# Performance work log

Hardware: AMD Instinct MI355X
Metric: run time of the kernel (lower is better)

The kernel has to match this reference:

```python
import jax, jax.numpy as jnp
import numpy as np

B, C_IN, C_OUT, H, W = 16, 128, 256, 80, 80
K, STRIDE, PAD = 3, 2, 1
KK = K * K
HO = (H + 2 * PAD - K) // STRIDE + 1
WO = (W + 2 * PAD - K) // STRIDE + 1


def setup_inputs() -> dict:
    key = jax.random.key(0)
    ks = jax.random.split(key, 3)
    x = jax.random.normal(ks[0], (B, C_IN, H, W), jnp.float32)
    offset_w = jax.random.normal(ks[1], (2 * KK, C_IN), jnp.float32) * 0.01
    offset_b = jnp.zeros((2 * KK,), jnp.float32)
    deform_w = jax.random.normal(ks[2], (C_OUT, C_IN, K, K), jnp.float32) * (1.0 / np.sqrt(C_IN * KK))
    deform_b = jnp.zeros((C_OUT,), jnp.float32)
    bn_gamma = jnp.ones((C_OUT,), jnp.float32)
    bn_beta = jnp.zeros((C_OUT,), jnp.float32)
    return dict(x=x, offset_w=offset_w, offset_b=offset_b, deform_w=deform_w,
                deform_b=deform_b, bn_gamma=bn_gamma, bn_beta=bn_beta)


def _bilinear_gather(x, py, px):
    # x: [B,C,H,W]; py,px: [B,KK,HO,WO] float sample coords; zero-pad outside.
    Bb, C, Hh, Ww = x.shape
    y0 = jnp.floor(py)
    x0 = jnp.floor(px)
    wy1 = py - y0
    wx1 = px - x0
    y0i = y0.astype(jnp.int32)
    x0i = x0.astype(jnp.int32)
    flat = x.reshape(Bb, C, Hh * Ww)

    def gather(yi, xi):
        valid = (yi >= 0) & (yi < Hh) & (xi >= 0) & (xi < Ww)
        idx = jnp.clip(yi, 0, Hh - 1) * Ww + jnp.clip(xi, 0, Ww - 1)
        g = jax.vmap(lambda f, i: f[:, i])(flat, idx.reshape(Bb, -1))
        g = g.reshape(Bb, C, *yi.shape[1:])
        return g * valid[:, None].astype(x.dtype)

    g00 = gather(y0i, x0i)
    g01 = gather(y0i, x0i + 1)
    g10 = gather(y0i + 1, x0i)
    g11 = gather(y0i + 1, x0i + 1)
    wy1 = wy1[:, None]  # [B,1,KK,HO,WO]
    wx1 = wx1[:, None]
    wy0 = 1.0 - wy1
    wx0 = 1.0 - wx1
    return wy0 * (wx0 * g00 + wx1 * g01) + wy1 * (wx0 * g10 + wx1 * g11)


def reference(x, offset_w, offset_b, deform_w, deform_b, bn_gamma, bn_beta):
    Bb = x.shape[0]
    # offset conv: 1x1, stride 2 (H,W even -> simple subsample)
    xs = x[:, :, ::2, ::2]  # [B,C,HO,WO]
    off = jnp.einsum('oc,bchw->bohw', offset_w, xs) + offset_b[None, :, None, None]
    off = off.reshape(Bb, KK, 2, HO, WO)  # torchvision layout: (dy,dx) per kernel tap
    dy, dx = off[:, :, 0], off[:, :, 1]
    ky = (jnp.arange(KK) // K).astype(jnp.float32)
    kx = (jnp.arange(KK) % K).astype(jnp.float32)
    base_y = (jnp.arange(HO) * STRIDE - PAD).astype(jnp.float32)
    base_x = (jnp.arange(WO) * STRIDE - PAD).astype(jnp.float32)
    py = base_y[None, None, :, None] + ky[None, :, None, None] + dy
    px = base_x[None, None, None, :] + kx[None, :, None, None] + dx
    sampled = _bilinear_gather(x, py, px)  # [B,C,KK,HO,WO]
    w = deform_w.reshape(C_OUT, C_IN * KK)
    out = jnp.einsum('ok,bkhw->bohw', w, sampled.reshape(Bb, C_IN * KK, HO, WO))
    out = out + deform_b[None, :, None, None]
    # BatchNorm2d in training mode (batch stats, biased var, eps=1e-5)
    mean = out.mean(axis=(0, 2, 3))
    var = out.var(axis=(0, 2, 3))
    out = (out - mean[None, :, None, None]) * jax.lax.rsqrt(var + 1e-5)[None, :, None, None]
    out = out * bn_gamma[None, :, None, None] + bn_beta[None, :, None, None]
    # SiLU
    return out * jax.nn.sigmoid(out)
```

## Files before the change

### kernel.cpp

```cpp
#include <hip/hip_runtime.h>
#include <hip/hip_bf16.h>

#define B_    16
#define CIN_  128
#define COUT_ 256
#define H_    80
#define W_    80
#define HO_   40
#define WO_   40
#define KK_   9
#define SK_   1152
#define NPIX_ 25600
#define NKS_  36

typedef __attribute__((ext_vector_type(8))) short short8;
typedef __attribute__((ext_vector_type(4))) float floatx4;

__device__ __forceinline__ unsigned short f2bu(float v) {
  __hip_bfloat16 h = __float2bfloat16(v);
  return *reinterpret_cast<unsigned short*>(&h);
}
__device__ __forceinline__ float bu2f(unsigned short u) {
  return __uint_as_float(((unsigned)u) << 16);
}
__device__ __forceinline__ unsigned int pk2(float a, float b) {
  return (unsigned)f2bu(a) | ((unsigned)f2bu(b) << 16);
}
__device__ __forceinline__ void gl_lds16(const unsigned short* g, unsigned short* l) {
  __builtin_amdgcn_global_load_lds(
      (const __attribute__((address_space(1))) unsigned int*)(const void*)g,
      (__attribute__((address_space(3))) unsigned int*)(void*)l, 16, 0, 0);
}

__global__ __launch_bounds__(256) void k_pack(const float* __restrict__ dw,
                                              unsigned short* __restrict__ Apk) {
  int t = blockIdx.x * 256 + threadIdx.x;
  int j  = t & 7;
  int sl = (t >> 3) & 3;
  int mh = (t >> 5) & 127;
  int cq = (t >> 12) & 1;
  int ks = t >> 13;
  int qd = (sl - (mh >> 1)) & 3;
  int m  = cq * 128 + mh;
  int k  = ks * 32 + qd * 8 + j;
  int kk = k >> 7, ci = k & 127;
  Apk[t] = f2bu(dw[m * SK_ + ci * KK_ + kk]);
}

__global__ __launch_bounds__(256) void k_cl(const float* __restrict__ x,
                                            const float* __restrict__ ow,
                                            const float* __restrict__ ob,
                                            unsigned short* __restrict__ xcl,
                                            float* __restrict__ off) {
  __shared__ unsigned int ts[CIN_ * 41];
  __shared__ float owl[18 * CIN_];
  __shared__ float obl[18];
  const int tid = threadIdx.x;
  const int bid = blockIdx.x;
  const int xcd = bid & 7;
  const int i0_ = bid >> 3;
  const int b   = (i0_ / 80) * 8 + xcd;
  const int y   = i0_ % 80;
  const bool even = (y & 1) == 0;

  for (int j = tid; j < CIN_ * 20; j += 256) {
    int ci = j / 20, xq = j % 20;
    float4 v = *(const float4*)&x[(((size_t)b * CIN_ + ci) * H_ + y) * W_ + xq * 4];
    ts[ci * 41 + xq * 2 + 0] = pk2(v.x, v.y);
    ts[ci * 41 + xq * 2 + 1] = pk2(v.z, v.w);
  }
  if (even) {
    for (int j = tid; j < 18 * CIN_; j += 256) owl[j] = ow[j];
    if (tid < 18) obl[tid] = ob[tid];
  }
  __syncthreads();

  unsigned short* op = xcl + ((size_t)b * H_ * W_ + (size_t)y * W_) * CIN_;
  for (int j = tid; j < 40 * 32; j += 256) {
    int xw = j >> 5, cg = j & 31;
    unsigned w0 = ts[(cg * 4 + 0) * 41 + xw];
    unsigned w1 = ts[(cg * 4 + 1) * 41 + xw];
    unsigned w2 = ts[(cg * 4 + 2) * 41 + xw];
    unsigned w3 = ts[(cg * 4 + 3) * 41 + xw];
    uint2 lo = make_uint2((w0 & 0xFFFFu) | (w1 << 16),
                          (w2 & 0xFFFFu) | (w3 << 16));
    uint2 hi = make_uint2((w0 >> 16) | (w1 & 0xFFFF0000u),
                          (w2 >> 16) | (w3 & 0xFFFF0000u));
    *(uint2*)(op + (size_t)(2 * xw) * CIN_ + cg * 4)     = lo;
    *(uint2*)(op + (size_t)(2 * xw + 1) * CIN_ + cg * 4) = hi;
  }

  if (even) {
    const int ho = y >> 1;
    for (int i = tid; i < 18 * WO_; i += 256) {
      int o = i / WO_, wo = i - o * WO_;
      float acc = obl[o];
      const float* wr = &owl[o * CIN_];
#pragma unroll 4
      for (int ci = 0; ci < CIN_; ci++)
        acc += wr[ci] * bu2f((unsigned short)(ts[ci * 41 + wo] & 0xFFFFu));
      off[((b * 18 + o) * HO_ + ho) * WO_ + wo] = acc;
    }
  }
}

__global__ __launch_bounds__(256) void k_sample_cl(const unsigned short* __restrict__ xcl,
                                                   const float* __restrict__ off,
                                                   unsigned short* __restrict__ Spk) {
  __shared__ __align__(16) int   pidx[80 * 4];
  __shared__ __align__(16) float pw[80 * 4];
  const int tid = threadIdx.x;
  const int j0   = blockIdx.x;
  const int xcd  = j0 & 7;
  const int s    = j0 >> 3;
  const int b_hi = s / 180;
  const int t0   = s % 180;
  const int g    = t0 / 9;
  const int kk   = t0 % 9;
  const int b    = b_hi * 8 + xcd;
  const int ho0  = g * 2;

  if (tid < 80) {
    int hop = tid / 40, px = tid % 40;
    int ho = ho0 + hop;
    float dy = off[((b * 18 + 2 * kk) * HO_ + ho) * WO_ + px];
    float dx = off[((b * 18 + 2 * kk + 1) * HO_ + ho) * WO_ + px];
    float py  = (float)(2 * ho - 1 + (kk / 3)) + dy;
    float pxf = (float)(2 * px - 1 + (kk % 3)) + dx;
    float y0f = floorf(py), x0f = floorf(pxf);
    float wy1 = py - y0f, wx1 = pxf - x0f;
    float wy0 = 1.f - wy1, wx0 = 1.f - wx1;
    int y0 = (int)y0f, x0 = (int)x0f;
    int y1 = y0 + 1, x1 = x0 + 1;
    bool vy0 = (y0 >= 0) && (y0 < H_);
    bool vy1 = (y1 >= 0) && (y1 < H_);
    bool vx0 = (x0 >= 0) && (x0 < W_);
    bool vx1 = (x1 >= 0) && (x1 < W_);
    int y0c = min(max(y0, 0), H_ - 1), y1c = min(max(y1, 0), H_ - 1);
    int x0c = min(max(x0, 0), W_ - 1), x1c = min(max(x1, 0), W_ - 1);
    pidx[tid * 4 + 0] = (y0c * W_ + x0c) << 7;  pw[tid * 4 + 0] = (vy0 && vx0) ? wy0 * wx0 : 0.f;
    pidx[tid * 4 + 1] = (y0c * W_ + x1c) << 7;  pw[tid * 4 + 1] = (vy0 && vx1) ? wy0 * wx1 : 0.f;
    pidx[tid * 4 + 2] = (y1c * W_ + x0c) << 7;  pw[tid * 4 + 2] = (vy1 && vx0) ? wy1 * wx0 : 0.f;
    pidx[tid * 4 + 3] = (y1c * W_ + x1c) << 7;  pw[tid * 4 + 3] = (vy1 && vx1) ? wy1 * wx1 : 0.f;
  }
  __syncthreads();

  const unsigned short* xb = xcl + (size_t)b * (H_ * W_ * CIN_);
#pragma unroll
  for (int it = 0; it < 5; it++) {
    int i = it * 256 + tid;
    int oct = i & 15;
    int pxh = i >> 4;
    int4   I  = *(const int4*)&pidx[pxh * 4];
    float4 Wv = *(const float4*)&pw[pxh * 4];
    short8 c00 = *(const short8*)(xb + I.x + oct * 8);
    short8 c01 = *(const short8*)(xb + I.y + oct * 8);
    short8 c10 = *(const short8*)(xb + I.z + oct * 8);
    short8 c11 = *(const short8*)(xb + I.w + oct * 8);
    short8 r;
#pragma unroll
    for (int i2 = 0; i2 < 8; i2++) {
      float v = Wv.x * bu2f((unsigned short)c00[i2]) +
                Wv.y * bu2f((unsigned short)c01[i2]) +
                Wv.z * bu2f((unsigned short)c10[i2]) +
                Wv.w * bu2f((unsigned short)c11[i2]);
      r[i2] = (short)f2bu(v);
    }
    int p  = b * 1600 + (ho0 + (pxh / 40)) * 40 + (pxh % 40);
    int pt = p >> 4, lm = p & 15;
    int ks = kk * 4 + (oct >> 2);
    int qd = oct & 3;
    int gr = lm * 4 + ((qd + (lm >> 1)) & 3);
    *(short8*)&Spk[(((size_t)pt * NKS_ + ks) * 64 + gr) * 8] = r;
  }
}

__global__ __launch_bounds__(256) void k_gemm(const unsigned short* __restrict__ Apk,
                                              const unsigned short* __restrict__ Spk,
                                              float* __restrict__ out,
                                              float* __restrict__ accum) {
  __shared__ __align__(16) unsigned short a_sh[3][4096];
  __shared__ __align__(16) unsigned short b_sh[3][4096];

  const int tid = threadIdx.x;
  const int wv = tid >> 6;
  const int ln = tid & 63;
  const int lm = ln & 15;
  const int qd = ln >> 4;
  const int wch = wv & 1;
  const int wpx = wv >> 1;

  const int bid = blockIdx.x;
  const int xcd = bid & 7;
  const int cq  = (bid >> 3) & 1;
  const int T   = bid >> 4;
  const int tile = T * 8 + xcd;
  const int pt0 = tile * 8;

  const unsigned short* ag = Apk + (size_t)cq * 4096 + (wv * 2) * 512 + ln * 8;
  const unsigned short* bg0 = Spk + ((size_t)(pt0 + wv * 2 + 0) * NKS_) * 512 + ln * 8;
  const unsigned short* bg1 = Spk + ((size_t)(pt0 + wv * 2 + 1) * NKS_) * 512 + ln * 8;

#define STAGE(t, bf) do {                                                  \
    gl_lds16(ag + (size_t)(t) * 8192,       &a_sh[bf][(wv * 2 + 0) * 512]);\
    gl_lds16(ag + (size_t)(t) * 8192 + 512, &a_sh[bf][(wv * 2 + 1) * 512]);\
    gl_lds16(bg0 + (size_t)(t) * 512,       &b_sh[bf][(wv * 2 + 0) * 512]);\
    gl_lds16(bg1 + (size_t)(t) * 512,       &b_sh[bf][(wv * 2 + 1) * 512]);\
  } while (0)

  floatx4 acc[4][4];
#pragma unroll
  for (int mt = 0; mt < 4; mt++)
#pragma unroll
    for (int nt = 0; nt < 4; nt++) acc[mt][nt] = (floatx4){0.f, 0.f, 0.f, 0.f};

  const int slot = (qd + (lm >> 1)) & 3;
  const int aoff0 = (wch * 64 + lm) * 32 + slot * 8;
  const int boff0 = (wpx * 4) * 512 + lm * 32 + slot * 8;

  STAGE(0, 0);
  STAGE(1, 1);
  asm volatile("s_waitcnt vmcnt(4)" ::: "memory");
  __builtin_amdgcn_s_barrier();

#pragma unroll 1
  for (int ks = 0; ks < NKS_; ks++) {
    const int bcur = ks % 3;
    if (ks + 2 < NKS_) STAGE(ks + 2, (ks + 2) % 3);

    short8 av[4], bv[4];
#pragma unroll
    for (int mt = 0; mt < 4; mt++)
      av[mt] = *(const short8*)(&a_sh[bcur][aoff0 + mt * 512]);
#pragma unroll
    for (int nt = 0; nt < 4; nt++)
      bv[nt] = *(const short8*)(&b_sh[bcur][boff0 + nt * 512]);
#pragma unroll
    for (int mt = 0; mt < 4; mt++)
#pragma unroll
      for (int nt = 0; nt < 4; nt++)
        acc[mt][nt] = __builtin_amdgcn_mfma_f32_16x16x32_bf16(av[mt], bv[nt],
                                                              acc[mt][nt], 0, 0, 0);
    if (ks + 1 < NKS_) {
      if (ks < NKS_ - 2) asm volatile("s_waitcnt vmcnt(4)" ::: "memory");
      else               asm volatile("s_waitcnt vmcnt(0)" ::: "memory");
      __builtin_amdgcn_s_barrier();
    }
  }
#undef STAGE

  const int cb0 = cq * 128 + wch * 64;
#pragma unroll
  for (int nt = 0; nt < 4; nt++) {
    const int p = (pt0 + wpx * 4 + nt) * 16 + lm;
    const int bb = p / 1600, rem = p - bb * 1600;
    float* ob = out + (size_t)bb * COUT_ * 1600 + rem;
#pragma unroll
    for (int mt = 0; mt < 4; mt++) {
#pragma unroll
      for (int r = 0; r < 4; r++)
        ob[(size_t)(cb0 + mt * 16 + qd * 4 + r) * 1600] = acc[mt][nt][r];
    }
  }

  __syncthreads();
  float* red = (float*)&a_sh[0][0];
  red[tid & 255] = 0.f;
  __syncthreads();
#pragma unroll
  for (int mt = 0; mt < 4; mt++) {
#pragma unroll
    for (int r = 0; r < 4; r++) {
      float s = acc[mt][0][r] + acc[mt][1][r] + acc[mt][2][r] + acc[mt][3][r];
      float q = acc[mt][0][r] * acc[mt][0][r] + acc[mt][1][r] * acc[mt][1][r] +
                acc[mt][2][r] * acc[mt][2][r] + acc[mt][3][r] * acc[mt][3][r];
#pragma unroll
      for (int d = 1; d < 16; d <<= 1) {
        s += __shfl_xor(s, d, 16);
        q += __shfl_xor(q, d, 16);
      }
      if (lm == 0) {
        int lc = wch * 64 + mt * 16 + qd * 4 + r;
        atomicAdd(&red[lc], s);
        atomicAdd(&red[128 + lc], q);
      }
    }
  }
  __syncthreads();
  if (tid < 128) {
    atomicAdd(&accum[cq * 128 + tid],         red[tid]);
    atomicAdd(&accum[COUT_ + cq * 128 + tid], red[128 + tid]);
  }
}

__global__ __launch_bounds__(256) void k_bn(float* __restrict__ io0,
                                            const float* __restrict__ accum,
                                            const float* __restrict__ gamma,
                                            const float* __restrict__ beta) {
  const int t = blockIdx.x * 256 + threadIdx.x;
  const int i0 = t * 4;
  const int c = (i0 / (HO_ * WO_)) % COUT_;
  const float mean = accum[c] * (1.f / NPIX_);
  const float var  = accum[COUT_ + c] * (1.f / NPIX_) - mean * mean;
  const float inv  = rsqrtf(var + 1e-5f);
  const float g  = gamma[c] * inv;
  const float be = beta[c] - mean * g;
  float4 r0 = *(const float4*)(io0 + i0);
  float v[4] = {r0.x, r0.y, r0.z, r0.w};
#pragma unroll
  for (int q = 0; q < 4; q++) {
    float u = v[q] * g + be;
    v[q] = u / (1.f + expf(-u));
  }
  *(float4*)(io0 + i0) = make_float4(v[0], v[1], v[2], v[3]);
}

extern "C" void kernel_launch(void* const* d_in, const int* in_sizes, int n_in,
                              void* d_out, int out_size, void* d_ws, size_t ws_size,
                              hipStream_t stream) {
  const float* x     = (const float*)d_in[0];
  const float* ow    = (const float*)d_in[1];
  const float* ob    = (const float*)d_in[2];
  const float* dw    = (const float*)d_in[3];
  const float* gamma = (const float*)d_in[5];
  const float* beta  = (const float*)d_in[6];
  float* out = (float*)d_out;

  float* off   = (float*)d_ws;
  float* accum = off + B_ * 18 * HO_ * WO_;
  unsigned short* Apk = (unsigned short*)(accum + 2 * COUT_);
  unsigned short* Spk = Apk + (size_t)SK_ * COUT_;
  unsigned short* xcl = Spk + (size_t)NPIX_ * SK_;

  hipMemsetAsync(accum, 0, 2 * COUT_ * sizeof(float), stream);
  k_pack<<<SK_, 256, 0, stream>>>(dw, Apk);
  k_cl<<<B_ * H_, 256, 0, stream>>>(x, ow, ob, xcl, off);
  k_sample_cl<<<B_ * KK_ * 20, 256, 0, stream>>>(xcl, off, Spk);
  k_gemm<<<400, 256, 0, stream>>>(Apk, Spk, out, accum);
  k_bn<<<(NPIX_ * COUT_ / 4 + 255) / 256, 256, 0, stream>>>(
      out, accum, gamma, beta);
}
```

Before: 185.5 us.

## Widen GEMM tile to all 256 output channels with 4-stage LDS pipeline

The GEMM block now covers all 256 output channels instead of splitting them across two blocks, so each sampled-column tile is loaded once and every wave computes 8x4 MFMA tiles. This halves the grid to 200 blocks, deepens the async global-to-LDS pipeline from 3 to 4 stages, and removes the XCD-aware tile mapping. The Spk layout drops its swizzle so B operands are read linearly, and the pack kernel is adjusted to the new A layout. In exchange it uses more registers and LDS per block and launches fewer blocks than there are CUs, which may reduce occupancy and leave some CUs idle.

```diff
diff --git a/kernel.cpp b/kernel.cpp
--- a/kernel.cpp
+++ b/kernel.cpp
@@ -37,11 +37,9 @@
   int t = blockIdx.x * 256 + threadIdx.x;
   int j  = t & 7;
   int sl = (t >> 3) & 3;
-  int mh = (t >> 5) & 127;
-  int cq = (t >> 12) & 1;
+  int m  = (t >> 5) & 255;
   int ks = t >> 13;
-  int qd = (sl - (mh >> 1)) & 3;
-  int m  = cq * 128 + mh;
+  int qd = (sl - (m >> 1)) & 3;
   int k  = ks * 32 + qd * 8 + j;
   int kk = k >> 7, ci = k & 127;
   Apk[t] = f2bu(dw[m * SK_ + ci * KK_ + kk]);
@@ -170,8 +168,7 @@
     int pt = p >> 4, lm = p & 15;
     int ks = kk * 4 + (oct >> 2);
     int qd = oct & 3;
-    int gr = lm * 4 + ((qd + (lm >> 1)) & 3);
-    *(short8*)&Spk[(((size_t)pt * NKS_ + ks) * 64 + gr) * 8] = r;
+    *(short8*)&Spk[(((size_t)pt * NKS_ + ks) * 64 + qd * 16 + lm) * 8] = r;
   }
 }
 
@@ -179,8 +176,8 @@
                                               const unsigned short* __restrict__ Spk,
                                               float* __restrict__ out,
                                               float* __restrict__ accum) {
-  __shared__ __align__(16) unsigned short a_sh[3][4096];
-  __shared__ __align__(16) unsigned short b_sh[3][4096];
+  __shared__ __align__(16) unsigned short a_sh[4][8192];
+  __shared__ __align__(16) unsigned short b_sh[4][4096];
 
   const int tid = threadIdx.x;
   const int wv = tid >> 6;
@@ -191,72 +188,70 @@
   const int wpx = wv >> 1;
 
   const int bid = blockIdx.x;
-  const int xcd = bid & 7;
-  const int cq  = (bid >> 3) & 1;
-  const int T   = bid >> 4;
-  const int tile = T * 8 + xcd;
-  const int pt0 = tile * 8;
-
-  const unsigned short* ag = Apk + (size_t)cq * 4096 + (wv * 2) * 512 + ln * 8;
-  const unsigned short* bg0 = Spk + ((size_t)(pt0 + wv * 2 + 0) * NKS_) * 512 + ln * 8;
-  const unsigned short* bg1 = Spk + ((size_t)(pt0 + wv * 2 + 1) * NKS_) * 512 + ln * 8;
-
-#define STAGE(t, bf) do {                                                  \
-    gl_lds16(ag + (size_t)(t) * 8192,       &a_sh[bf][(wv * 2 + 0) * 512]);\
-    gl_lds16(ag + (size_t)(t) * 8192 + 512, &a_sh[bf][(wv * 2 + 1) * 512]);\
-    gl_lds16(bg0 + (size_t)(t) * 512,       &b_sh[bf][(wv * 2 + 0) * 512]);\
-    gl_lds16(bg1 + (size_t)(t) * 512,       &b_sh[bf][(wv * 2 + 1) * 512]);\
+  const int pt0 = bid * 8;
+
+  const unsigned short* ag = Apk + wv * 2048 + ln * 8;
+  const unsigned short* bg = Spk + ln * 8;
+
+#define STAGE(t, bf) do {                                                       \
+    gl_lds16(ag + (size_t)(t) * 8192 + 0 * 512, &a_sh[bf][wv * 2048 + 0 * 512]);\
+    gl_lds16(ag + (size_t)(t) * 8192 + 1 * 512, &a_sh[bf][wv * 2048 + 1 * 512]);\
+    gl_lds16(ag + (size_t)(t) * 8192 + 2 * 512, &a_sh[bf][wv * 2048 + 2 * 512]);\
+    gl_lds16(ag + (size_t)(t) * 8192 + 3 * 512, &a_sh[bf][wv * 2048 + 3 * 512]);\
+    gl_lds16(bg + ((size_t)(pt0 + wv * 2 + 0) * NKS_ + (t)) * 512,              \
+             &b_sh[bf][wv * 1024 + 0 * 512]);                                   \
+    gl_lds16(bg + ((size_t)(pt0 + wv * 2 + 1) * NKS_ + (t)) * 512,              \
+             &b_sh[bf][wv * 1024 + 1 * 512]);                                   \
   } while (0)
 
-  floatx4 acc[4][4];
-#pragma unroll
-  for (int mt = 0; mt < 4; mt++)
+  floatx4 acc[8][4];
+#pragma unroll
+  for (int mt = 0; mt < 8; mt++)
 #pragma unroll
     for (int nt = 0; nt < 4; nt++) acc[mt][nt] = (floatx4){0.f, 0.f, 0.f, 0.f};
 
-  const int slot = (qd + (lm >> 1)) & 3;
-  const int aoff0 = (wch * 64 + lm) * 32 + slot * 8;
-  const int boff0 = (wpx * 4) * 512 + lm * 32 + slot * 8;
+  const int slot  = (qd + (lm >> 1)) & 3;
+  const int abase = (wch * 128 + lm) * 32 + slot * 8;
+  const int bbase = (wpx * 4) * 512 + ln * 8;
 
   STAGE(0, 0);
   STAGE(1, 1);
-  asm volatile("s_waitcnt vmcnt(4)" ::: "memory");
-  __builtin_amdgcn_s_barrier();
+  STAGE(2, 2);
 
 #pragma unroll 1
   for (int ks = 0; ks < NKS_; ks++) {
-    const int bcur = ks % 3;
-    if (ks + 2 < NKS_) STAGE(ks + 2, (ks + 2) % 3);
-
-    short8 av[4], bv[4];
-#pragma unroll
-    for (int mt = 0; mt < 4; mt++)
-      av[mt] = *(const short8*)(&a_sh[bcur][aoff0 + mt * 512]);
-#pragma unroll
-    for (int nt = 0; nt < 4; nt++)
-      bv[nt] = *(const short8*)(&b_sh[bcur][boff0 + nt * 512]);
-#pragma unroll
-    for (int mt = 0; mt < 4; mt++)
+    if (ks < NKS_ - 2)       asm volatile("s_waitcnt vmcnt(12)" ::: "memory");
+    else if (ks == NKS_ - 2) asm volatile("s_waitcnt vmcnt(6)" ::: "memory");
+    else                     asm volatile("s_waitcnt vmcnt(0)" ::: "memory");
+    __builtin_amdgcn_s_barrier();
+    if (ks + 3 < NKS_) STAGE(ks + 3, (ks + 3) & 3);
+
+    const unsigned short* al = &a_sh[ks & 3][abase];
+    const unsigned short* bl = &b_sh[ks & 3][bbase];
+    short8 av[8], bv[4];
+#pragma unroll
+    for (int mt = 0; mt < 8; mt++) av[mt] = *(const short8*)(al + mt * 512);
+#pragma unroll
+    for (int nt = 0; nt < 4; nt++) bv[nt] = *(const short8*)(bl + nt * 512);
+#pragma unroll
+    for (int mt = 0; mt < 8; mt++)
 #pragma unroll
       for (int nt = 0; nt < 4; nt++)
         acc[mt][nt] = __builtin_amdgcn_mfma_f32_16x16x32_bf16(av[mt], bv[nt],
                                                               acc[mt][nt], 0, 0, 0);
-    if (ks + 1 < NKS_) {
-      if (ks < NKS_ - 2) asm volatile("s_waitcnt vmcnt(4)" ::: "memory");
-      else               asm volatile("s_waitcnt vmcnt(0)" ::: "memory");
-      __builtin_amdgcn_s_barrier();
-    }
+    asm volatile("s_waitcnt lgkmcnt(0)" ::: "memory");
   }
 #undef STAGE
 
-  const int cb0 = cq * 128 + wch * 64;
+  const int cb0 = wch * 128;
 #pragma unroll
   for (int nt = 0; nt < 4; nt++) {
-    const int p = (pt0 + wpx * 4 + nt) * 16 + lm;
-    const int bb = p / 1600, rem = p - bb * 1600;
+    const int pt = pt0 + wpx * 4 + nt;
+    const int bb = pt / 100;
+    const int rem = (pt - bb * 100) * 16 + lm;
     float* ob = out + (size_t)bb * COUT_ * 1600 + rem;
 #pragma unroll
-    for (int mt = 0; mt < 4; mt++) {
+    for (int mt = 0; mt < 8; mt++) {
 #pragma unroll
       for (int r = 0; r < 4; r++)
         ob[(size_t)(cb0 + mt * 16 + qd * 4 + r) * 1600] = acc[mt][nt][r];
@@ -265,10 +260,10 @@
 
   __syncthreads();
   float* red = (float*)&a_sh[0][0];
-  red[tid & 255] = 0.f;
-  __syncthreads();
-#pragma unroll
-  for (int mt = 0; mt < 4; mt++) {
+  if (tid < 256) { red[tid] = 0.f; red[256 + tid] = 0.f; }
+  __syncthreads();
+#pragma unroll
+  for (int mt = 0; mt < 8; mt++) {
 #pragma unroll
     for (int r = 0; r < 4; r++) {
       float s = acc[mt][0][r] + acc[mt][1][r] + acc[mt][2][r] + acc[mt][3][r];
@@ -280,16 +275,16 @@
         q += __shfl_xor(q, d, 16);
       }
       if (lm == 0) {
-        int lc = wch * 64 + mt * 16 + qd * 4 + r;
+        int lc = cb0 + mt * 16 + qd * 4 + r;
         atomicAdd(&red[lc], s);
-        atomicAdd(&red[128 + lc], q);
+        atomicAdd(&red[256 + lc], q);
       }
     }
   }
   __syncthreads();
-  if (tid < 128) {
-    atomicAdd(&accum[cq * 128 + tid],         red[tid]);
-    atomicAdd(&accum[COUT_ + cq * 128 + tid], red[128 + tid]);
+  if (tid < 256) {
+    atomicAdd(&accum[tid],         red[tid]);
+    atomicAdd(&accum[COUT_ + tid], red[256 + tid]);
   }
 }
 
@@ -336,7 +331,7 @@
   k_pack<<<SK_, 256, 0, stream>>>(dw, Apk);
   k_cl<<<B_ * H_, 256, 0, stream>>>(x, ow, ob, xcl, off);
   k_sample_cl<<<B_ * KK_ * 20, 256, 0, stream>>>(xcl, off, Spk);
-  k_gemm<<<400, 256, 0, stream>>>(Apk, Spk, out, accum);
+  k_gemm<<<200, 256, 0, stream>>>(Apk, Spk, out, accum);
   k_bn<<<(NPIX_ * COUT_ / 4 + 255) / 256, 256, 0, stream>>>(
       out, accum, gamma, beta);
 }
```

After: 198.2 us. 6.9% more time.
